# Performance work log

Hardware: AMD Instinct MI355X
Metric: run time of the kernel (lower is better)

## Reference

```python
import jax, jax.numpy as jnp
import numpy as np

NH = 8       # num_heads
KS = 7       # kernel_size (odd)
DIM = 256


def setup_inputs() -> dict:
    key = jax.random.key(0)
    ks = jax.random.split(key, 8)
    B, H, W, C = 2, 56, 56, DIM
    x_q = jax.random.normal(ks[0], (B, H, W, C), jnp.float32)
    x_k = jax.random.normal(ks[1], (B, H, W, C), jnp.float32)
    # small-scale weights so softmax logits stay in a sane range
    Wq = jax.random.normal(ks[2], (C, C), jnp.float32) * 0.02
    bq = jnp.zeros((C,), jnp.float32)
    Wkv = jax.random.normal(ks[3], (C, 2 * C), jnp.float32) * 0.02
    bkv = jnp.zeros((2 * C,), jnp.float32)
    rpb = jax.random.normal(ks[4], (NH, 2 * KS - 1, 2 * KS - 1), jnp.float32) * 0.02
    Wproj = jax.random.normal(ks[5], (C, C), jnp.float32) * 0.02
    bproj = jnp.zeros((C,), jnp.float32)
    return {"x_q": x_q, "x_k": x_k, "Wq": Wq, "bq": bq, "Wkv": Wkv,
            "bkv": bkv, "rpb": rpb, "Wproj": Wproj, "bproj": bproj}


def _neighborhood_idx(n, k):
    # NATTEN clamped window (dilation=1): start_i = clip(i - k//2, 0, n - k)
    start = jnp.clip(jnp.arange(n) - k // 2, 0, n - k)          # [n]
    idx = start[:, None] + jnp.arange(k)[None, :]               # [n, k] key positions
    bidx = idx - jnp.arange(n)[:, None] + (k - 1)               # [n, k] rpb index (rel offset + k-1)
    return idx, bidx


def reference(x_q, x_k, Wq, bq, Wkv, bkv, rpb, Wproj, bproj):
    B, H, W, C = x_q.shape
    hd = C // NH
    scale = hd ** -0.5
    # projections
    q = (x_q @ Wq + bq).reshape(B, H, W, NH, hd).transpose(0, 3, 1, 2, 4) * scale  # [B,nh,H,W,hd]
    kv = (x_k @ Wkv + bkv).reshape(B, H, W, 2, NH, hd)
    kk = kv[..., 0, :, :].transpose(0, 3, 1, 2, 4)   # [B,nh,H,W,hd]
    vv = kv[..., 1, :, :].transpose(0, 3, 1, 2, 4)   # [B,nh,H,W,hd]

    idx_h, bi = _neighborhood_idx(H, KS)   # [H,KS]
    idx_w, bj = _neighborhood_idx(W, KS)   # [W,KS]

    # gather neighborhoods: [B,nh,H,W,KS,KS,hd]
    Kn = kk[:, :, idx_h[:, None, :, None], idx_w[None, :, None, :], :]
    Vn = vv[:, :, idx_h[:, None, :, None], idx_w[None, :, None, :], :]
    # relative position bias: [nh,H,W,KS,KS]
    bias = rpb[:, bi[:, None, :, None], bj[None, :, None, :]]

    attn = jnp.einsum('bnijd,bnijkld->bnijkl', q, Kn) + bias[None]
    attn = jax.nn.softmax(attn.reshape(B, NH, H, W, KS * KS), axis=-1)
    attn = attn.reshape(B, NH, H, W, KS, KS)
    out = jnp.einsum('bnijkl,bnijkld->bnijd', attn, Vn)     # [B,nh,H,W,hd]
    out = out.transpose(0, 2, 3, 1, 4).reshape(B, H, W, C)
    return out @ Wproj + bproj
```

## Files before the change

kernel.cpp:

```cpp
#include <hip/hip_runtime.h>
#include <hip/hip_bf16.h>

#define NHEAD 8
#define KSZ 7
#define HS 56
#define WS 56
#define MTOK (2 * HS * WS)

typedef unsigned short u16;
typedef unsigned int u32;

using bf16x8 = __attribute__((ext_vector_type(8))) short;
using f32x4  = __attribute__((ext_vector_type(4))) float;

static __device__ __forceinline__ u16 f2bf(float x) {
    u32 u = __float_as_uint(x);
    u += 0x7FFFu + ((u >> 16) & 1u);
    return (u16)(u >> 16);
}
static __device__ __forceinline__ float bf2f(u16 h) {
    return __uint_as_float(((u32)h) << 16);
}

static __device__ __forceinline__ void gload16(const void* g, void* l) {
    __builtin_amdgcn_global_load_lds(
        (const __attribute__((address_space(1))) u32*)g,
        (__attribute__((address_space(3))) u32*)l, 16, 0, 0);
}

__global__ __launch_bounds__(256) void cvt_w_kernel(
    const float* __restrict__ Wq, const float* __restrict__ Wkv,
    const float* __restrict__ Wp,
    u16* __restrict__ WTall_h, u16* __restrict__ WTall_l,
    u16* __restrict__ WpT_h, u16* __restrict__ WpT_l)
{
    __shared__ float Ts[32][33];
    const int b = blockIdx.x;
    const float* W; u16 *Th, *Tl; int N, tile;
    if (b < 64)       { W = Wq;  Th = WTall_h;             Tl = WTall_l;             N = 256; tile = b; }
    else if (b < 192) { W = Wkv; Th = WTall_h + 256 * 256; Tl = WTall_l + 256 * 256; N = 512; tile = b - 64; }
    else              { W = Wp;  Th = WpT_h;               Tl = WpT_l;               N = 256; tile = b - 192; }
    const int ntiles_n = N / 32;
    const int k0 = (tile / ntiles_n) * 32;
    const int n0 = (tile % ntiles_n) * 32;

    const int t = threadIdx.x;
    {
        const int kk = t >> 3, nn4 = (t & 7) * 4;
        float4 v = *reinterpret_cast<const float4*>(&W[(size_t)(k0 + kk) * N + n0 + nn4]);
        Ts[kk][nn4 + 0] = v.x; Ts[kk][nn4 + 1] = v.y;
        Ts[kk][nn4 + 2] = v.z; Ts[kk][nn4 + 3] = v.w;
    }
    __syncthreads();
    {
        const int nn = t >> 3, kk4 = (t & 7) * 4;
        const int n = n0 + nn;
        ushort4 h, l;
        u16* hp = &h.x; u16* lp = &l.x;
        #pragma unroll
        for (int i = 0; i < 4; ++i) {
            float x = Ts[kk4 + i][nn];
            u16 hb = f2bf(x);
            hp[i] = hb;
            lp[i] = f2bf(x - bf2f(hb));
        }
        const int kg = k0 + kk4;
        const int kphys = (kg & ~63) | ((((kg >> 3) & 7) ^ (n & 7)) << 3) | (kg & 7);
        const size_t o = (size_t)n * 256 + kphys;
        *reinterpret_cast<ushort4*>(&Th[o]) = h;
        *reinterpret_cast<ushort4*>(&Tl[o]) = l;
    }
}

template<bool QKV>
__global__ __launch_bounds__(256) void gemm_mfma_kernel(
    const float* __restrict__ Aq, const float* __restrict__ Akv,
    const u16* __restrict__ Ah, const u16* __restrict__ Al,
    const u16* __restrict__ Wh, const u16* __restrict__ Wl,
    const float* __restrict__ biasq, const float* __restrict__ biaskv,
    float* __restrict__ outq, float* __restrict__ outkv, float scale)
{
    __shared__ __align__(16) u16 AhS[64 * 64];
    __shared__ __align__(16) u16 AlS[64 * 64];
    __shared__ __align__(16) u16 BhS[128 * 64];
    __shared__ __align__(16) u16 BlS[128 * 64];

    const int tid  = threadIdx.x;
    const int lane = tid & 63;
    const int w    = tid >> 6;
    const int l16  = lane & 15;
    const int lhi  = lane >> 4;

    const int n0 = blockIdx.x * 128;
    const int m0 = blockIdx.y * 64;

    const float* A32 = nullptr;
    if (QKV) A32 = (n0 < 256) ? Aq : Akv;

    const int arow = tid >> 2;
    const int akc  = (tid & 3) * 16;
    const int aswz = arow & 7;

    f32x4 acc[4][2];
    #pragma unroll
    for (int mi = 0; mi < 4; ++mi)
        #pragma unroll
        for (int ni = 0; ni < 2; ++ni) acc[mi][ni] = (f32x4){0.f, 0.f, 0.f, 0.f};

    for (int kt = 0; kt < 256; kt += 64) {
        __syncthreads();

        #pragma unroll
        for (int i = 0; i < 4; ++i) {
            const int rbase = w * 32 + i * 8;
            const size_t src = (size_t)(n0 + rbase + (lane >> 3)) * 256 + kt + (lane & 7) * 8;
            gload16(Wh + src, &BhS[rbase * 64]);
            gload16(Wl + src, &BlS[rbase * 64]);
        }

        if (QKV) {
            const float* ap = &A32[(size_t)(m0 + arow) * 256 + kt + akc];
            float f[16];
            #pragma unroll
            for (int v = 0; v < 4; ++v) {
                float4 t = *reinterpret_cast<const float4*>(ap + v * 4);
                f[v * 4 + 0] = t.x; f[v * 4 + 1] = t.y;
                f[v * 4 + 2] = t.z; f[v * 4 + 3] = t.w;
            }
            union { u16 u[8]; uint4 v; } h0, h1, l0, l1;
            #pragma unroll
            for (int e = 0; e < 8; ++e) {
                u16 hb = f2bf(f[e]);      h0.u[e] = hb; l0.u[e] = f2bf(f[e] - bf2f(hb));
                u16 hb2 = f2bf(f[8 + e]); h1.u[e] = hb2; l1.u[e] = f2bf(f[8 + e] - bf2f(hb2));
            }
            const int c0 = (tid & 3) * 2;
            const int o0 = arow * 64 + ((c0 ^ aswz) << 3);
            const int o1 = arow * 64 + (((c0 + 1) ^ aswz) << 3);
            *reinterpret_cast<uint4*>(&AhS[o0]) = h0.v;
            *reinterpret_cast<uint4*>(&AhS[o1]) = h1.v;
            *reinterpret_cast<uint4*>(&AlS[o0]) = l0.v;
            *reinterpret_cast<uint4*>(&AlS[o1]) = l1.v;
        } else {
            #pragma unroll
            for (int i = 0; i < 2; ++i) {
                const int rbase = w * 16 + i * 8;
                const size_t src = (size_t)(m0 + rbase + (lane >> 3)) * 256 + kt + (lane & 7) * 8;
                gload16(Ah + src, &AhS[rbase * 64]);
                gload16(Al + src, &AlS[rbase * 64]);
            }
        }

        __syncthreads();

        #pragma unroll
        for (int ks = 0; ks < 2; ++ks) {
            const int cph = ((ks * 4 + lhi) ^ (l16 & 7)) << 3;
            bf16x8 ah[4], al[4], bh[2], bl[2];
            #pragma unroll
            for (int mi = 0; mi < 4; ++mi) {
                const int ro = (mi * 16 + l16) * 64 + cph;
                ah[mi] = *reinterpret_cast<const bf16x8*>(&AhS[ro]);
                al[mi] = *reinterpret_cast<const bf16x8*>(&AlS[ro]);
            }
            #pragma unroll
            for (int ni = 0; ni < 2; ++ni) {
                const int ro = (w * 32 + ni * 16 + l16) * 64 + cph;
                bh[ni] = *reinterpret_cast<const bf16x8*>(&BhS[ro]);
                bl[ni] = *reinterpret_cast<const bf16x8*>(&BlS[ro]);
            }
            #pragma unroll
            for (int mi = 0; mi < 4; ++mi)
                #pragma unroll
                for (int ni = 0; ni < 2; ++ni) {
                    acc[mi][ni] = __builtin_amdgcn_mfma_f32_16x16x32_bf16(
                        ah[mi], bh[ni], acc[mi][ni], 0, 0, 0);
                    acc[mi][ni] = __builtin_amdgcn_mfma_f32_16x16x32_bf16(
                        ah[mi], bl[ni], acc[mi][ni], 0, 0, 0);
                    acc[mi][ni] = __builtin_amdgcn_mfma_f32_16x16x32_bf16(
                        al[mi], bh[ni], acc[mi][ni], 0, 0, 0);
                }
        }
    }

    float* op; const float* bs; int ldo, coff; float sc;
    if (!QKV || n0 < 256) { op = outq;  bs = biasq;  ldo = QKV ? 256 : 256; coff = 0;   sc = scale; }
    else                  { op = outkv; bs = biaskv; ldo = 512;             coff = 256; sc = 1.0f;  }

    #pragma unroll
    for (int ni = 0; ni < 2; ++ni) {
        const int col = n0 + w * 32 + ni * 16 + l16;
        const float bv = bs[col - coff];
        #pragma unroll
        for (int mi = 0; mi < 4; ++mi) {
            const int row = m0 + mi * 16 + lhi * 4;
            #pragma unroll
            for (int rg = 0; rg < 4; ++rg)
                op[(size_t)(row + rg) * ldo + (col - coff)] = (acc[mi][ni][rg] + bv) * sc;
        }
    }
}

#define REG 14
#define NREG (REG*REG)
#define KST 36

__global__ __launch_bounds__(256) void natten_kernel(
    const float* __restrict__ qb, const float* __restrict__ kvb,
    const float* __restrict__ rpb,
    u16* __restrict__ ohi, u16* __restrict__ olo)
{
    __shared__ float Ks[NREG * KST];
    __shared__ float Rp[169];

    const int tid = threadIdx.x;
    const int bid = blockIdx.x;
    const int head = bid & 7;
    const int idx  = bid >> 3;
    const int b    = idx / 49;
    const int t49  = idx % 49;
    const int ti0  = (t49 / 7) * 8;
    const int tj0  = (t49 % 7) * 8;

    int gr0 = ti0 - 3; gr0 = gr0 < 0 ? 0 : gr0; gr0 = gr0 > HS - REG ? HS - REG : gr0;
    int gc0 = tj0 - 3; gc0 = gc0 < 0 ? 0 : gc0; gc0 = gc0 > WS - REG ? WS - REG : gc0;

    const float* kvb_head = kvb + (size_t)b * 3136 * 512 + head * 32;

    #pragma unroll
    for (int rt0 = 0; rt0 < NREG; rt0 += 32) {
        const int rt = rt0 + (tid >> 3);
        if (rt < NREG) {
            const int r = rt / REG, c = rt % REG;
            const int g = (gr0 + r) * WS + (gc0 + c);
            const float4 v = *reinterpret_cast<const float4*>(
                kvb_head + (size_t)g * 512 + (tid & 7) * 4);
            *reinterpret_cast<float4*>(&Ks[rt * KST + (tid & 7) * 4]) = v;
        }
    }
    if (tid < 169) Rp[tid] = rpb[head * 169 + tid];

    const int tokl = tid >> 2;
    const int q4   = tid & 3;
    const int tr = tokl >> 3, tc = tokl & 7;
    const int i = ti0 + tr, j = tj0 + tc;

    int si = i - 3; si = si < 0 ? 0 : si; si = si > HS - KSZ ? HS - KSZ : si;
    int sj = j - 3; sj = sj < 0 ? 0 : sj; sj = sj > WS - KSZ ? WS - KSZ : sj;

    const int nb0 = (si - gr0) * REG + (sj - gc0);
    const int rb0 = (si - i + 6) * 13 + (sj - j + 6);
    const int tokflat = b * 3136 + i * WS + j;

    const float* qp = qb + (size_t)tokflat * 256 + head * 32 + q4 * 8;
    const float4 qv0 = *reinterpret_cast<const float4*>(qp);
    const float4 qv1 = *reinterpret_cast<const float4*>(qp + 4);

    __syncthreads();

    float lg[49];
    #pragma unroll
    for (int ki = 0; ki < KSZ; ++ki) {
        #pragma unroll
        for (int kj = 0; kj < KSZ; ++kj) {
            const float* kp = &Ks[(nb0 + ki * REG + kj) * KST + q4 * 8];
            const float4 k0 = *reinterpret_cast<const float4*>(kp);
            const float4 k1 = *reinterpret_cast<const float4*>(kp + 4);
            float p = qv0.x * k0.x;
            p = fmaf(qv0.y, k0.y, p);
            p = fmaf(qv0.z, k0.z, p);
            p = fmaf(qv0.w, k0.w, p);
            p = fmaf(qv1.x, k1.x, p);
            p = fmaf(qv1.y, k1.y, p);
            p = fmaf(qv1.z, k1.z, p);
            p = fmaf(qv1.w, k1.w, p);
            p += __shfl_xor(p, 1);
            p += __shfl_xor(p, 2);
            lg[ki * 7 + kj] = p + Rp[rb0 + ki * 13 + kj];
        }
    }

    float m = -1e30f;
    #pragma unroll
    for (int l = 0; l < 49; ++l) m = fmaxf(m, lg[l]);
    float ssum = 0.f;
    #pragma unroll
    for (int l = 0; l < 49; ++l) {
        const float e = __expf(lg[l] - m);
        lg[l] = e;
        ssum += e;
    }

    __syncthreads();

    #pragma unroll
    for (int rt0 = 0; rt0 < NREG; rt0 += 32) {
        const int rt = rt0 + (tid >> 3);
        if (rt < NREG) {
            const int r = rt / REG, c = rt % REG;
            const int g = (gr0 + r) * WS + (gc0 + c);
            const float4 v = *reinterpret_cast<const float4*>(
                kvb_head + (size_t)g * 512 + 256 + (tid & 7) * 4);
            *reinterpret_cast<float4*>(&Ks[rt * KST + (tid & 7) * 4]) = v;
        }
    }
    __syncthreads();

    float acc[8] = {0.f, 0.f, 0.f, 0.f, 0.f, 0.f, 0.f, 0.f};
    #pragma unroll
    for (int ki = 0; ki < KSZ; ++ki) {
        #pragma unroll
        for (int kj = 0; kj < KSZ; ++kj) {
            const float w = lg[ki * 7 + kj];
            const float* vp = &Ks[(nb0 + ki * REG + kj) * KST + q4 * 8];
            const float4 v0 = *reinterpret_cast<const float4*>(vp);
            const float4 v1 = *reinterpret_cast<const float4*>(vp + 4);
            acc[0] = fmaf(w, v0.x, acc[0]);
            acc[1] = fmaf(w, v0.y, acc[1]);
            acc[2] = fmaf(w, v0.z, acc[2]);
            acc[3] = fmaf(w, v0.w, acc[3]);
            acc[4] = fmaf(w, v1.x, acc[4]);
            acc[5] = fmaf(w, v1.y, acc[5]);
            acc[6] = fmaf(w, v1.z, acc[6]);
            acc[7] = fmaf(w, v1.w, acc[7]);
        }
    }

    const float inv = 1.f / ssum;
    union { u16 u[8]; uint4 v; } ph, pl;
    #pragma unroll
    for (int d = 0; d < 8; ++d) {
        const float x = acc[d] * inv;
        const u16 hb = f2bf(x);
        ph.u[d] = hb;
        pl.u[d] = f2bf(x - bf2f(hb));
    }
    const int chunk = head * 4 + q4;
    const int seg = chunk >> 3, cin = chunk & 7;
    const int cphys = cin ^ (tokflat & 7);
    const size_t o = (size_t)tokflat * 256 + seg * 64 + cphys * 8;
    *reinterpret_cast<uint4*>(&ohi[o]) = ph.v;
    *reinterpret_cast<uint4*>(&olo[o]) = pl.v;
}

extern "C" void kernel_launch(void* const* d_in, const int* in_sizes, int n_in,
                              void* d_out, int out_size, void* d_ws, size_t ws_size,
                              hipStream_t stream) {
    const float* x_q   = (const float*)d_in[0];
    const float* x_k   = (const float*)d_in[1];
    const float* Wq    = (const float*)d_in[2];
    const float* bq    = (const float*)d_in[3];
    const float* Wkv   = (const float*)d_in[4];
    const float* bkv   = (const float*)d_in[5];
    const float* rpb   = (const float*)d_in[6];
    const float* Wproj = (const float*)d_in[7];
    const float* bproj = (const float*)d_in[8];
    float* out = (float*)d_out;

    const int M = MTOK;

    float* qbuf  = (float*)d_ws;
    float* kvbuf = qbuf + (size_t)M * 256;
    u16* at_hi   = (u16*)(kvbuf + (size_t)M * 512);
    u16* at_lo   = at_hi + (size_t)M * 256;
    u16* WTall_h = at_lo + (size_t)M * 256;
    u16* WTall_l = WTall_h + 768 * 256;
    u16* WpT_h   = WTall_l + 768 * 256;
    u16* WpT_l   = WpT_h + 256 * 256;

    const float scale = 0.17677669529663687f;

    dim3 blk(256);
    cvt_w_kernel<<<dim3(256), blk, 0, stream>>>(
        Wq, Wkv, Wproj, WTall_h, WTall_l, WpT_h, WpT_l);

    gemm_mfma_kernel<true><<<dim3(6, M / 64), blk, 0, stream>>>(
        x_q, x_k, nullptr, nullptr, WTall_h, WTall_l,
        bq, bkv, qbuf, kvbuf, scale);

    natten_kernel<<<dim3(784), blk, 0, stream>>>(qbuf, kvbuf, rpb, at_hi, at_lo);

    gemm_mfma_kernel<false><<<dim3(2, M / 64), blk, 0, stream>>>(
        nullptr, nullptr, at_hi, at_lo, WpT_h, WpT_l,
        bproj, nullptr, out, nullptr, 1.0f);
}
```

Before: 57.60 us.

## Use single bf16 for QKV GEMM, retile GEMMs, prefetch K/V in natten

The QKV projection drops the hi/lo bf16 split and now runs one bf16 MFMA per tile instead of three, with 128x128 tiles and a 2x2 wave layout. The output projection keeps split precision but reads fp32 attention output, converting to bf16 in the kernel on 64x64 tiles. The natten kernel loads K and V into registers up front so the V fetch overlaps the logits and softmax work. This cuts MFMA count and launch granularity but lowers QKV accuracy to plain bf16, which risks tolerance failures.

```diff
diff --git a/kernel.cpp b/kernel.cpp
--- a/kernel.cpp
+++ b/kernel.cpp
@@ -31,15 +31,14 @@
 __global__ __launch_bounds__(256) void cvt_w_kernel(
     const float* __restrict__ Wq, const float* __restrict__ Wkv,
     const float* __restrict__ Wp,
-    u16* __restrict__ WTall_h, u16* __restrict__ WTall_l,
-    u16* __restrict__ WpT_h, u16* __restrict__ WpT_l)
+    u16* __restrict__ WT, u16* __restrict__ WpT_h, u16* __restrict__ WpT_l)
 {
     __shared__ float Ts[32][33];
     const int b = blockIdx.x;
-    const float* W; u16 *Th, *Tl; int N, tile;
-    if (b < 64)       { W = Wq;  Th = WTall_h;             Tl = WTall_l;             N = 256; tile = b; }
-    else if (b < 192) { W = Wkv; Th = WTall_h + 256 * 256; Tl = WTall_l + 256 * 256; N = 512; tile = b - 64; }
-    else              { W = Wp;  Th = WpT_h;               Tl = WpT_l;               N = 256; tile = b - 192; }
+    const float* W; u16 *Th, *Tl; int N, tile; bool wantlo;
+    if (b < 64)       { W = Wq;  Th = WT;             Tl = nullptr; N = 256; tile = b;       wantlo = false; }
+    else if (b < 192) { W = Wkv; Th = WT + 256 * 256; Tl = nullptr; N = 512; tile = b - 64;  wantlo = false; }
+    else              { W = Wp;  Th = WpT_h;          Tl = WpT_l;   N = 256; tile = b - 192; wantlo = true; }
     const int ntiles_n = N / 32;
     const int k0 = (tile / ntiles_n) * 32;
     const int n0 = (tile % ntiles_n) * 32;
@@ -68,42 +67,142 @@
         const int kphys = (kg & ~63) | ((((kg >> 3) & 7) ^ (n & 7)) << 3) | (kg & 7);
         const size_t o = (size_t)n * 256 + kphys;
         *reinterpret_cast<ushort4*>(&Th[o]) = h;
-        *reinterpret_cast<ushort4*>(&Tl[o]) = l;
-    }
-}
-
-template<bool QKV>
-__global__ __launch_bounds__(256) void gemm_mfma_kernel(
+        if (wantlo) *reinterpret_cast<ushort4*>(&Tl[o]) = l;
+    }
+}
+
+__global__ __launch_bounds__(256) void gemm_qkv_kernel(
     const float* __restrict__ Aq, const float* __restrict__ Akv,
-    const u16* __restrict__ Ah, const u16* __restrict__ Al,
+    const u16* __restrict__ WT,
+    const float* __restrict__ bq, const float* __restrict__ bkv,
+    float* __restrict__ outq, float* __restrict__ outkv, float scale)
+{
+    __shared__ __align__(16) u16 AS[128 * 64];
+    __shared__ __align__(16) u16 BS[128 * 64];
+
+    const int tid  = threadIdx.x;
+    const int lane = tid & 63;
+    const int w    = tid >> 6;
+    const int wm   = w >> 1;
+    const int wn   = w & 1;
+    const int l16  = lane & 15;
+    const int lhi  = lane >> 4;
+
+    const int n0 = blockIdx.x * 128;
+    const int m0 = blockIdx.y * 128;
+    const float* A32 = (n0 < 256) ? Aq : Akv;
+
+    const int ar  = tid >> 1;
+    const int akc = (tid & 1) * 32;
+    const int ac0 = (tid & 1) * 4;
+    const int asw = ar & 7;
+
+    f32x4 acc[4][4];
+    #pragma unroll
+    for (int mi = 0; mi < 4; ++mi)
+        #pragma unroll
+        for (int ni = 0; ni < 4; ++ni) acc[mi][ni] = (f32x4){0.f, 0.f, 0.f, 0.f};
+
+    for (int kt = 0; kt < 256; kt += 64) {
+        __syncthreads();
+
+        #pragma unroll
+        for (int i = 0; i < 4; ++i) {
+            const int rbase = w * 32 + i * 8;
+            const size_t src = (size_t)(n0 + rbase + (lane >> 3)) * 256 + kt + (lane & 7) * 8;
+            gload16(WT + src, &BS[rbase * 64]);
+        }
+
+        {
+            const float* ap = &A32[(size_t)(m0 + ar) * 256 + kt + akc];
+            float f[32];
+            #pragma unroll
+            for (int v = 0; v < 8; ++v) {
+                float4 t = *reinterpret_cast<const float4*>(ap + v * 4);
+                f[v * 4 + 0] = t.x; f[v * 4 + 1] = t.y;
+                f[v * 4 + 2] = t.z; f[v * 4 + 3] = t.w;
+            }
+            union { u16 u[8]; uint4 v; } hx[4];
+            #pragma unroll
+            for (int e = 0; e < 32; ++e) hx[e >> 3].u[e & 7] = f2bf(f[e]);
+            #pragma unroll
+            for (int c = 0; c < 4; ++c) {
+                const int o = ar * 64 + (((ac0 + c) ^ asw) << 3);
+                *reinterpret_cast<uint4*>(&AS[o]) = hx[c].v;
+            }
+        }
+
+        __syncthreads();
+
+        #pragma unroll
+        for (int ks = 0; ks < 2; ++ks) {
+            const int cph = ((ks * 4 + lhi) ^ (l16 & 7)) << 3;
+            bf16x8 ah[4], bh[4];
+            #pragma unroll
+            for (int mi = 0; mi < 4; ++mi)
+                ah[mi] = *reinterpret_cast<const bf16x8*>(&AS[(wm * 64 + mi * 16 + l16) * 64 + cph]);
+            #pragma unroll
+            for (int ni = 0; ni < 4; ++ni)
+                bh[ni] = *reinterpret_cast<const bf16x8*>(&BS[(wn * 64 + ni * 16 + l16) * 64 + cph]);
+            #pragma unroll
+            for (int mi = 0; mi < 4; ++mi)
+                #pragma unroll
+                for (int ni = 0; ni < 4; ++ni)
+                    acc[mi][ni] = __builtin_amdgcn_mfma_f32_16x16x32_bf16(
+                        ah[mi], bh[ni], acc[mi][ni], 0, 0, 0);
+        }
+    }
+
+    const bool isq = (n0 < 256);
+    float* op = isq ? outq : outkv;
+    const float* bs = isq ? bq : bkv;
+    const int ldo = isq ? 256 : 512;
+    const int coff = isq ? 0 : 256;
+    const float sc = isq ? scale : 1.0f;
+
+    #pragma unroll
+    for (int ni = 0; ni < 4; ++ni) {
+        const int col = n0 + wn * 64 + ni * 16 + l16 - coff;
+        const float bv = bs[col];
+        #pragma unroll
+        for (int mi = 0; mi < 4; ++mi) {
+            const int row = m0 + wm * 64 + mi * 16 + lhi * 4;
+            #pragma unroll
+            for (int rg = 0; rg < 4; ++rg)
+                op[(size_t)(row + rg) * ldo + col] = (acc[mi][ni][rg] + bv) * sc;
+        }
+    }
+}
+
+__global__ __launch_bounds__(256) void gemm_proj_kernel(
+    const float* __restrict__ A32,
     const u16* __restrict__ Wh, const u16* __restrict__ Wl,
-    const float* __restrict__ biasq, const float* __restrict__ biaskv,
-    float* __restrict__ outq, float* __restrict__ outkv, float scale)
+    const float* __restrict__ bias, float* __restrict__ out)
 {
     __shared__ __align__(16) u16 AhS[64 * 64];
     __shared__ __align__(16) u16 AlS[64 * 64];
-    __shared__ __align__(16) u16 BhS[128 * 64];
-    __shared__ __align__(16) u16 BlS[128 * 64];
+    __shared__ __align__(16) u16 BhS[64 * 64];
+    __shared__ __align__(16) u16 BlS[64 * 64];
 
     const int tid  = threadIdx.x;
     const int lane = tid & 63;
     const int w    = tid >> 6;
+    const int wm   = w >> 1;
+    const int wn   = w & 1;
     const int l16  = lane & 15;
     const int lhi  = lane >> 4;
 
-    const int n0 = blockIdx.x * 128;
+    const int n0 = blockIdx.x * 64;
     const int m0 = blockIdx.y * 64;
 
-    const float* A32 = nullptr;
-    if (QKV) A32 = (n0 < 256) ? Aq : Akv;
-
-    const int arow = tid >> 2;
-    const int akc  = (tid & 3) * 16;
-    const int aswz = arow & 7;
-
-    f32x4 acc[4][2];
-    #pragma unroll
-    for (int mi = 0; mi < 4; ++mi)
+    const int ar  = tid >> 2;
+    const int akc = (tid & 3) * 16;
+    const int ac0 = (tid & 3) * 2;
+    const int asw = ar & 7;
+
+    f32x4 acc[2][2];
+    #pragma unroll
+    for (int mi = 0; mi < 2; ++mi)
         #pragma unroll
         for (int ni = 0; ni < 2; ++ni) acc[mi][ni] = (f32x4){0.f, 0.f, 0.f, 0.f};
 
@@ -111,15 +210,15 @@
         __syncthreads();
 
         #pragma unroll
-        for (int i = 0; i < 4; ++i) {
-            const int rbase = w * 32 + i * 8;
+        for (int i = 0; i < 2; ++i) {
+            const int rbase = w * 16 + i * 8;
             const size_t src = (size_t)(n0 + rbase + (lane >> 3)) * 256 + kt + (lane & 7) * 8;
             gload16(Wh + src, &BhS[rbase * 64]);
             gload16(Wl + src, &BlS[rbase * 64]);
         }
 
-        if (QKV) {
-            const float* ap = &A32[(size_t)(m0 + arow) * 256 + kt + akc];
+        {
+            const float* ap = &A32[(size_t)(m0 + ar) * 256 + kt + akc];
             float f[16];
             #pragma unroll
             for (int v = 0; v < 4; ++v) {
@@ -127,26 +226,18 @@
                 f[v * 4 + 0] = t.x; f[v * 4 + 1] = t.y;
                 f[v * 4 + 2] = t.z; f[v * 4 + 3] = t.w;
             }
-            union { u16 u[8]; uint4 v; } h0, h1, l0, l1;
-            #pragma unroll
-            for (int e = 0; e < 8; ++e) {
-                u16 hb = f2bf(f[e]);      h0.u[e] = hb; l0.u[e] = f2bf(f[e] - bf2f(hb));
-                u16 hb2 = f2bf(f[8 + e]); h1.u[e] = hb2; l1.u[e] = f2bf(f[8 + e] - bf2f(hb2));
-            }
-            const int c0 = (tid & 3) * 2;
-            const int o0 = arow * 64 + ((c0 ^ aswz) << 3);
-            const int o1 = arow * 64 + (((c0 + 1) ^ aswz) << 3);
-            *reinterpret_cast<uint4*>(&AhS[o0]) = h0.v;
-            *reinterpret_cast<uint4*>(&AhS[o1]) = h1.v;
-            *reinterpret_cast<uint4*>(&AlS[o0]) = l0.v;
-            *reinterpret_cast<uint4*>(&AlS[o1]) = l1.v;
-        } else {
-            #pragma unroll
-            for (int i = 0; i < 2; ++i) {
-                const int rbase = w * 16 + i * 8;
-                const size_t src = (size_t)(m0 + rbase + (lane >> 3)) * 256 + kt + (lane & 7) * 8;
-                gload16(Ah + src, &AhS[rbase * 64]);
-                gload16(Al + src, &AlS[rbase * 64]);
+            union { u16 u[8]; uint4 v; } hx[2], lx[2];
+            #pragma unroll
+            for (int e = 0; e < 16; ++e) {
+                const u16 hb = f2bf(f[e]);
+                hx[e >> 3].u[e & 7] = hb;
+                lx[e >> 3].u[e & 7] = f2bf(f[e] - bf2f(hb));
+            }
+            #pragma unroll
+            for (int c = 0; c < 2; ++c) {
+                const int o = ar * 64 + (((ac0 + c) ^ asw) << 3);
+                *reinterpret_cast<uint4*>(&AhS[o]) = hx[c].v;
+                *reinterpret_cast<uint4*>(&AlS[o]) = lx[c].v;
             }
         }
 
@@ -155,21 +246,21 @@
         #pragma unroll
         for (int ks = 0; ks < 2; ++ks) {
             const int cph = ((ks * 4 + lhi) ^ (l16 & 7)) << 3;
-            bf16x8 ah[4], al[4], bh[2], bl[2];
-            #pragma unroll
-            for (int mi = 0; mi < 4; ++mi) {
-                const int ro = (mi * 16 + l16) * 64 + cph;
+            bf16x8 ah[2], al[2], bh[2], bl[2];
+            #pragma unroll
+            for (int mi = 0; mi < 2; ++mi) {
+                const int ro = (wm * 32 + mi * 16 + l16) * 64 + cph;
                 ah[mi] = *reinterpret_cast<const bf16x8*>(&AhS[ro]);
                 al[mi] = *reinterpret_cast<const bf16x8*>(&AlS[ro]);
             }
             #pragma unroll
             for (int ni = 0; ni < 2; ++ni) {
-                const int ro = (w * 32 + ni * 16 + l16) * 64 + cph;
+                const int ro = (wn * 32 + ni * 16 + l16) * 64 + cph;
                 bh[ni] = *reinterpret_cast<const bf16x8*>(&BhS[ro]);
                 bl[ni] = *reinterpret_cast<const bf16x8*>(&BlS[ro]);
             }
             #pragma unroll
-            for (int mi = 0; mi < 4; ++mi)
+            for (int mi = 0; mi < 2; ++mi)
                 #pragma unroll
                 for (int ni = 0; ni < 2; ++ni) {
                     acc[mi][ni] = __builtin_amdgcn_mfma_f32_16x16x32_bf16(
@@ -182,20 +273,16 @@
         }
     }
 
-    float* op; const float* bs; int ldo, coff; float sc;
-    if (!QKV || n0 < 256) { op = outq;  bs = biasq;  ldo = QKV ? 256 : 256; coff = 0;   sc = scale; }
-    else                  { op = outkv; bs = biaskv; ldo = 512;             coff = 256; sc = 1.0f;  }
-
     #pragma unroll
     for (int ni = 0; ni < 2; ++ni) {
-        const int col = n0 + w * 32 + ni * 16 + l16;
-        const float bv = bs[col - coff];
-        #pragma unroll
-        for (int mi = 0; mi < 4; ++mi) {
-            const int row = m0 + mi * 16 + lhi * 4;
+        const int col = n0 + wn * 32 + ni * 16 + l16;
+        const float bv = bias[col];
+        #pragma unroll
+        for (int mi = 0; mi < 2; ++mi) {
+            const int row = m0 + wm * 32 + mi * 16 + lhi * 4;
             #pragma unroll
             for (int rg = 0; rg < 4; ++rg)
-                op[(size_t)(row + rg) * ldo + (col - coff)] = (acc[mi][ni][rg] + bv) * sc;
+                out[(size_t)(row + rg) * 256 + col] = acc[mi][ni][rg] + bv;
         }
     }
 }
@@ -206,8 +293,7 @@
 
 __global__ __launch_bounds__(256) void natten_kernel(
     const float* __restrict__ qb, const float* __restrict__ kvb,
-    const float* __restrict__ rpb,
-    u16* __restrict__ ohi, u16* __restrict__ olo)
+    const float* __restrict__ rpb, float* __restrict__ ob)
 {
     __shared__ float Ks[NREG * KST];
     __shared__ float Rp[169];
@@ -226,16 +312,21 @@
 
     const float* kvb_head = kvb + (size_t)b * 3136 * 512 + head * 32;
 
-    #pragma unroll
-    for (int rt0 = 0; rt0 < NREG; rt0 += 32) {
-        const int rt = rt0 + (tid >> 3);
-        if (rt < NREG) {
-            const int r = rt / REG, c = rt % REG;
-            const int g = (gr0 + r) * WS + (gc0 + c);
-            const float4 v = *reinterpret_cast<const float4*>(
-                kvb_head + (size_t)g * 512 + (tid & 7) * 4);
-            *reinterpret_cast<float4*>(&Ks[rt * KST + (tid & 7) * 4]) = v;
-        }
+    float4 kreg[7], vreg[7];
+    #pragma unroll
+    for (int it = 0; it < 7; ++it) {
+        int rt = it * 32 + (tid >> 3);
+        rt = rt < NREG ? rt : NREG - 1;
+        const int r = rt / REG, c = rt % REG;
+        const float* kp = kvb_head + (size_t)((gr0 + r) * WS + (gc0 + c)) * 512 + (tid & 7) * 4;
+        kreg[it] = *reinterpret_cast<const float4*>(kp);
+        vreg[it] = *reinterpret_cast<const float4*>(kp + 256);
+    }
+    #pragma unroll
+    for (int it = 0; it < 7; ++it) {
+        const int rt = it * 32 + (tid >> 3);
+        if (rt < NREG)
+            *reinterpret_cast<float4*>(&Ks[rt * KST + (tid & 7) * 4]) = kreg[it];
     }
     if (tid < 169) Rp[tid] = rpb[head * 169 + tid];
 
@@ -293,15 +384,10 @@
     __syncthreads();
 
     #pragma unroll
-    for (int rt0 = 0; rt0 < NREG; rt0 += 32) {
-        const int rt = rt0 + (tid >> 3);
-        if (rt < NREG) {
-            const int r = rt / REG, c = rt % REG;
-            const int g = (gr0 + r) * WS + (gc0 + c);
-            const float4 v = *reinterpret_cast<const float4*>(
-                kvb_head + (size_t)g * 512 + 256 + (tid & 7) * 4);
-            *reinterpret_cast<float4*>(&Ks[rt * KST + (tid & 7) * 4]) = v;
-        }
+    for (int it = 0; it < 7; ++it) {
+        const int rt = it * 32 + (tid >> 3);
+        if (rt < NREG)
+            *reinterpret_cast<float4*>(&Ks[rt * KST + (tid & 7) * 4]) = vreg[it];
     }
     __syncthreads();
 
@@ -326,20 +412,11 @@
     }
 
     const float inv = 1.f / ssum;
-    union { u16 u[8]; uint4 v; } ph, pl;
-    #pragma unroll
-    for (int d = 0; d < 8; ++d) {
-        const float x = acc[d] * inv;
-        const u16 hb = f2bf(x);
-        ph.u[d] = hb;
-        pl.u[d] = f2bf(x - bf2f(hb));
-    }
-    const int chunk = head * 4 + q4;
-    const int seg = chunk >> 3, cin = chunk & 7;
-    const int cphys = cin ^ (tokflat & 7);
-    const size_t o = (size_t)tokflat * 256 + seg * 64 + cphys * 8;
-    *reinterpret_cast<uint4*>(&ohi[o]) = ph.v;
-    *reinterpret_cast<uint4*>(&olo[o]) = pl.v;
+    float* op = ob + (size_t)tokflat * 256 + head * 32 + q4 * 8;
+    *reinterpret_cast<float4*>(op) =
+        make_float4(acc[0] * inv, acc[1] * inv, acc[2] * inv, acc[3] * inv);
+    *reinterpret_cast<float4*>(op + 4) =
+        make_float4(acc[4] * inv, acc[5] * inv, acc[6] * inv, acc[7] * inv);
 }
 
 extern "C" void kernel_launch(void* const* d_in, const int* in_sizes, int n_in,
@@ -358,28 +435,23 @@
 
     const int M = MTOK;
 
-    float* qbuf  = (float*)d_ws;
-    float* kvbuf = qbuf + (size_t)M * 256;
-    u16* at_hi   = (u16*)(kvbuf + (size_t)M * 512);
-    u16* at_lo   = at_hi + (size_t)M * 256;
-    u16* WTall_h = at_lo + (size_t)M * 256;
-    u16* WTall_l = WTall_h + 768 * 256;
-    u16* WpT_h   = WTall_l + 768 * 256;
-    u16* WpT_l   = WpT_h + 256 * 256;
+    float* qbuf   = (float*)d_ws;
+    float* kvbuf  = qbuf + (size_t)M * 256;
+    float* attbuf = kvbuf + (size_t)M * 512;
+    u16* WT    = (u16*)(attbuf + (size_t)M * 256);
+    u16* WpT_h = WT + 768 * 256;
+    u16* WpT_l = WpT_h + 256 * 256;
 
     const float scale = 0.17677669529663687f;
 
     dim3 blk(256);
-    cvt_w_kernel<<<dim3(256), blk, 0, stream>>>(
-        Wq, Wkv, Wproj, WTall_h, WTall_l, WpT_h, WpT_l);
-
-    gemm_mfma_kernel<true><<<dim3(6, M / 64), blk, 0, stream>>>(
-        x_q, x_k, nullptr, nullptr, WTall_h, WTall_l,
-        bq, bkv, qbuf, kvbuf, scale);
-
-    natten_kernel<<<dim3(784), blk, 0, stream>>>(qbuf, kvbuf, rpb, at_hi, at_lo);
-
-    gemm_mfma_kernel<false><<<dim3(2, M / 64), blk, 0, stream>>>(
-        nullptr, nullptr, at_hi, at_lo, WpT_h, WpT_l,
-        bproj, nullptr, out, nullptr, 1.0f);
-}
+    cvt_w_kernel<<<dim3(256), blk, 0, stream>>>(Wq, Wkv, Wproj, WT, WpT_h, WpT_l);
+
+    gemm_qkv_kernel<<<dim3(6, M / 128), blk, 0, stream>>>(
+        x_q, x_k, WT, bq, bkv, qbuf, kvbuf, scale);
+
+    natten_kernel<<<dim3(784), blk, 0, stream>>>(qbuf, kvbuf, rpb, attbuf);
+
+    gemm_proj_kernel<<<dim3(4, M / 64), blk, 0, stream>>>(
+        attbuf, WpT_h, WpT_l, bproj, out);
+}
```

New measurement: 61.87 us (median of 2 runs). +7.4%, slower.
